# Performance work log

Hardware: AMD Instinct MI355X
Metric: run time of the kernel (lower is better)

Reference implementation:

```python
import jax, jax.numpy as jnp
import numpy as np

B, S, F, D, H, L = 32, 512, 40, 512, 8, 4
T = S + 1
DK, DV = D // 2, D          # expand_k=0.5, expand_v=1.0 (fla GLA defaults)
HK, HV = DK // H, DV // H
GLR = 16                    # gate low-rank dim
GLN = 16.0                  # gate logit normalizer
MLP = 4 * D


def sin_pos(t, d, n=10000.0):
    pos = jnp.arange(t, dtype=jnp.float32)[:, None]
    den = jnp.power(n, 2.0 * jnp.arange(d // 2, dtype=jnp.float32) / d)
    e = jnp.zeros((t, d), jnp.float32)
    e = e.at[:, 0::2].set(jnp.sin(pos / den))
    e = e.at[:, 1::2].set(jnp.cos(pos / den))
    return e


def layernorm(x, w, b, eps=1e-5):
    m = x.mean(-1, keepdims=True)
    v = ((x - m) ** 2).mean(-1, keepdims=True)
    return (x - m) * jax.lax.rsqrt(v + eps) * w + b


def bin_norm(x, l1, b1, l2, b2, y1, y2):
    # x: (b, f, s). BiN: temporal z-norm with per-feature affine (X2) +
    # feature z-norm with per-time affine (X1); unbiased std, small std -> 1.
    st = jnp.sqrt(x.var(axis=2, ddof=1, keepdims=True))
    st = jnp.where(st < 1e-4, 1.0, st)
    Z2 = (x - x.mean(axis=2, keepdims=True)) / st
    X2 = l2[None, :, None] * Z2 + b2[None, :, None]
    sf = jnp.sqrt(x.var(axis=1, ddof=1, keepdims=True))
    sf = jnp.where(sf < 1e-4, 1.0, sf)
    Z1 = (x - x.mean(axis=1, keepdims=True)) / sf
    X1 = l1[None, None, :] * Z1 + b1[None, None, :]
    return y1 * X1 + y2 * X2


def gla_attn(x, qw, kw, vw, gw, gkw1, gkw2, gkb2, gnw, ow):
    # Gated linear attention, recurrent form: S_t = exp(gk_t) * S_{t-1} + k_t v_t^T
    b, t, _ = x.shape
    q = (x @ qw).reshape(b, t, H, HK) * (HK ** -0.5)
    k = (x @ kw).reshape(b, t, H, HK)
    v = (x @ vw).reshape(b, t, H, HV)
    g = (x @ gw).reshape(b, t, H, HV)
    gk = (jax.nn.log_sigmoid((x @ gkw1) @ gkw2 + gkb2) / GLN).reshape(b, t, H, HK)

    def step(Sc, inp):
        qt, kt, vt, gt = inp                       # (b,H,HK),(b,H,HK),(b,H,HV),(b,H,HK)
        Sc = Sc * jnp.exp(gt)[..., None] + kt[..., None] * vt[..., None, :]
        return Sc, jnp.einsum('bhk,bhkv->bhv', qt, Sc)

    init = jnp.zeros((b, H, HK, HV), x.dtype)
    to_t = lambda a: jnp.swapaxes(a, 0, 1)        # (t, b, H, dim)
    _, o = jax.lax.scan(step, init, (to_t(q), to_t(k), to_t(v), to_t(gk)))
    o = jnp.swapaxes(o, 0, 1)                     # (b, t, H, HV)
    o = o * jax.lax.rsqrt((o * o).mean(-1, keepdims=True) + 1e-5) * gnw  # head RMSNorm
    o = o * g * jax.nn.sigmoid(g)                 # swish output gate
    return o.reshape(b, t, DV) @ ow


def setup_inputs():
    key = jax.random.key(0)
    ks = iter(jax.random.split(key, 64))
    r = lambda shape, s=0.02: jax.random.normal(next(ks), shape, jnp.float32) * s
    return dict(
        x=jax.random.normal(next(ks), (B, S, F), jnp.float32),
        bin_l1=r((S,), 0.1), bin_b1=jnp.zeros((S,), jnp.float32),
        bin_l2=r((F,), 0.1), bin_b2=jnp.zeros((F,), jnp.float32),
        bin_y1=jnp.float32(0.5), bin_y2=jnp.float32(0.5),
        emb_w=r((F, D)), emb_b=jnp.zeros((D,), jnp.float32),
        cls_token=jnp.zeros((D,), jnp.float32),
        ln1_w=jnp.ones((L, D), jnp.float32), ln1_b=jnp.zeros((L, D), jnp.float32),
        q_w=r((L, D, DK)), k_w=r((L, D, DK)), v_w=r((L, D, DV)), g_w=r((L, D, DV)),
        gk_w1=r((L, D, GLR)), gk_w2=r((L, GLR, DK)), gk_b2=jnp.zeros((L, DK), jnp.float32),
        gnorm_w=jnp.ones((L, HV), jnp.float32),
        o_w=r((L, DV, D)),
        ln2_w=jnp.ones((L, D), jnp.float32), ln2_b=jnp.zeros((L, D), jnp.float32),
        mlp_w1=r((L, D, MLP)), mlp_b1=jnp.zeros((L, MLP), jnp.float32),
        mlp_w2=r((L, MLP, D)), mlp_b2=jnp.zeros((L, D), jnp.float32),
        head_w=r((D, 3)), head_b=jnp.zeros((3,), jnp.float32),
    )


def reference(x, bin_l1, bin_b1, bin_l2, bin_b2, bin_y1, bin_y2, emb_w, emb_b,
              cls_token, ln1_w, ln1_b, q_w, k_w, v_w, g_w, gk_w1, gk_w2, gk_b2,
              gnorm_w, o_w, ln2_w, ln2_b, mlp_w1, mlp_b1, mlp_w2, mlp_b2,
              head_w, head_b):
    h = bin_norm(jnp.swapaxes(x, 1, 2), bin_l1, bin_b1, bin_l2, bin_b2, bin_y1, bin_y2)
    h = jnp.swapaxes(h, 1, 2) @ emb_w + emb_b                    # (b, s, D)
    cls = jnp.broadcast_to(cls_token, (h.shape[0], 1, D))
    h = jnp.concatenate([h, cls], axis=1) + sin_pos(T, D)[None]  # (b, s+1, D)
    for i in range(L):
        a = gla_attn(layernorm(h, ln1_w[i], ln1_b[i]), q_w[i], k_w[i], v_w[i],
                     g_w[i], gk_w1[i], gk_w2[i], gk_b2[i], gnorm_w[i], o_w[i])
        h = h + a
        m = layernorm(h, ln2_w[i], ln2_b[i])
        m = jax.nn.gelu(m @ mlp_w1[i] + mlp_b1[i], approximate=False)
        h = h + m @ mlp_w2[i] + mlp_b2[i]
    return h[:, -1] @ head_w + head_b                            # (b, 3)
```

## Files before the change

### kernel.cpp

```cpp
#include <hip/hip_runtime.h>
#include <hip/hip_bf16.h>
#include <hip/hip_fp16.h>
#include <math.h>

#define Bsz   32
#define Ssz   512
#define Fsz   40
#define Dsz   512
#define Hh    8
#define Lnum  4
#define Tsz   513
#define DKsz  256
#define DVsz  512
#define HKsz  32
#define HVsz  64
#define Msz   (Bsz*Tsz)
#define Mpad  16512
#define MLPsz 2048
#define NCH   16
#define CSZ   33
#define QKVG  1536
#define VOFFH 8404992

typedef __attribute__((ext_vector_type(4))) float f32x4;
typedef __attribute__((ext_vector_type(8))) short bf16x8;

__device__ __forceinline__ float bf2f(short s) {
  unsigned int u = ((unsigned int)(unsigned short)s) << 16;
  return __builtin_bit_cast(float, u);
}
__device__ __forceinline__ short f2bf(float f) {
  __hip_bfloat16 b = __float2bfloat16(f);
  return __builtin_bit_cast(short, b);
}

__device__ __forceinline__ float wave_sum(float v) {
#pragma unroll
  for (int off = 32; off > 0; off >>= 1) v += __shfl_xor(v, off, 64);
  return v;
}

__global__ void pos_kernel(float* __restrict__ pos) {
  int idx = blockIdx.x * 256 + threadIdx.x;
  if (idx >= Tsz * Dsz) return;
  int t = idx / Dsz, d = idx % Dsz;
  float e = (float)(2 * (d >> 1)) / (float)Dsz;
  float den = powf(10000.f, e);
  float a = (float)t / den;
  pos[idx] = (d & 1) ? cosf(a) : sinf(a);
}

__global__ void tstat_kernel(const float* __restrict__ x,
                             float* __restrict__ mt, float* __restrict__ rst) {
  int bf = blockIdx.x;
  int b = bf / Fsz, f = bf % Fsz;
  int lane = threadIdx.x;
  const float* xp = x + (size_t)b * Ssz * Fsz + f;
  float s = 0.f, sq = 0.f;
  for (int i = lane; i < Ssz; i += 64) {
    float v = xp[(size_t)i * Fsz];
    s += v; sq += v * v;
  }
  s = wave_sum(s); sq = wave_sum(sq);
  if (lane == 0) {
    float m = s / (float)Ssz;
    float var = (sq - (float)Ssz * m * m) / (float)(Ssz - 1);
    float st = sqrtf(fmaxf(var, 0.f));
    if (st < 1e-4f) st = 1.f;
    mt[bf] = m;
    rst[bf] = 1.f / st;
  }
}

__global__ __launch_bounds__(64) void binorm_kernel(
    const float* __restrict__ x, const float* __restrict__ l1,
    const float* __restrict__ b1, const float* __restrict__ l2,
    const float* __restrict__ b2, const float* __restrict__ y1p,
    const float* __restrict__ y2p, const float* __restrict__ mt,
    const float* __restrict__ rst, float* __restrict__ xbT) {
  int row = blockIdx.x;
  int lane = threadIdx.x;
  int b = row / Tsz, t = row % Tsz;
  bool valid = (row < Msz) && (t < Ssz);
  if (!valid) {
    if (lane < Fsz) xbT[(size_t)lane * Mpad + row] = 0.f;
    return;
  }
  float xv = 0.f;
  const float* xp = x + ((size_t)b * Ssz + t) * Fsz;
  if (lane < Fsz) xv = xp[lane];
  float s  = wave_sum(lane < Fsz ? xv : 0.f);
  float sq = wave_sum(lane < Fsz ? xv * xv : 0.f);
  float m = s / (float)Fsz;
  float var = (sq - (float)Fsz * m * m) / (float)(Fsz - 1);
  float sf = sqrtf(fmaxf(var, 0.f));
  if (sf < 1e-4f) sf = 1.f;
  if (lane < Fsz) {
    float y1 = y1p[0], y2 = y2p[0];
    float z1 = (xv - m) / sf;
    float X1 = l1[t] * z1 + b1[t];
    int bf = b * Fsz + lane;
    float z2 = (xv - mt[bf]) * rst[bf];
    float X2 = l2[lane] * z2 + b2[lane];
    xbT[(size_t)lane * Mpad + row] = y1 * X1 + y2 * X2;
  }
}

__global__ __launch_bounds__(256, 4) void embgemm_kernel(
    const float* __restrict__ xbT, const float* __restrict__ emb_w,
    const float* __restrict__ emb_b, const float* __restrict__ cls,
    const float* __restrict__ pos, float* __restrict__ h) {
  __shared__ float as[Fsz][64];
  __shared__ float bs[Fsz][64];
  int tid = threadIdx.x, tx = tid & 15, ty = tid >> 4;
  int r0 = blockIdx.x * 64, c0 = blockIdx.y * 64;
  for (int idx = tid; idx < Fsz * 64; idx += 256) {
    int f = idx >> 6, r = idx & 63;
    as[f][r] = xbT[(size_t)f * Mpad + r0 + r];
    bs[f][r] = emb_w[f * Dsz + c0 + r];
  }
  __syncthreads();
  float acc[4][4] = {};
#pragma unroll 5
  for (int f = 0; f < Fsz; ++f) {
    float4 a = *(const float4*)&as[f][ty * 4];
    float4 bv = *(const float4*)&bs[f][tx * 4];
    float av[4] = {a.x, a.y, a.z, a.w};
    float bw[4] = {bv.x, bv.y, bv.z, bv.w};
#pragma unroll
    for (int i = 0; i < 4; ++i)
#pragma unroll
      for (int j = 0; j < 4; ++j) acc[i][j] += av[i] * bw[j];
  }
#pragma unroll
  for (int i = 0; i < 4; ++i) {
    int gm = r0 + ty * 4 + i;
    int t = gm % Tsz;
    const float* pp = pos + (size_t)t * Dsz;
    bool iscls = (t == Ssz);
    int gn = c0 + tx * 4;
#pragma unroll
    for (int j = 0; j < 4; ++j) {
      float v = iscls ? (cls[gn + j] + pp[gn + j])
                      : (acc[i][j] + emb_b[gn + j] + pp[gn + j]);
      h[(size_t)gm * Dsz + gn + j] = v;
    }
  }
}

__global__ __launch_bounds__(64) void ln_kernel(
    const float* __restrict__ in, const float* __restrict__ w,
    const float* __restrict__ b, short* __restrict__ out) {
  int row = blockIdx.x, lane = threadIdx.x;
  const float* p = in + (size_t)row * Dsz;
  float4 v0 = *(const float4*)(p + lane * 8);
  float4 v1 = *(const float4*)(p + lane * 8 + 4);
  float s  = v0.x + v0.y + v0.z + v0.w + v1.x + v1.y + v1.z + v1.w;
  float sq = v0.x*v0.x + v0.y*v0.y + v0.z*v0.z + v0.w*v0.w
           + v1.x*v1.x + v1.y*v1.y + v1.z*v1.z + v1.w*v1.w;
  s = wave_sum(s); sq = wave_sum(sq);
  float m = s * (1.f / Dsz);
  float var = sq * (1.f / Dsz) - m * m;
  float r = rsqrtf(var + 1e-5f);
  float4 w0 = *(const float4*)(w + lane * 8);
  float4 w1 = *(const float4*)(w + lane * 8 + 4);
  float4 b0 = *(const float4*)(b + lane * 8);
  float4 b1v = *(const float4*)(b + lane * 8 + 4);
  bf16x8 pk;
  pk[0] = f2bf((v0.x - m) * r * w0.x + b0.x);
  pk[1] = f2bf((v0.y - m) * r * w0.y + b0.y);
  pk[2] = f2bf((v0.z - m) * r * w0.z + b0.z);
  pk[3] = f2bf((v0.w - m) * r * w0.w + b0.w);
  pk[4] = f2bf((v1.x - m) * r * w1.x + b1v.x);
  pk[5] = f2bf((v1.y - m) * r * w1.y + b1v.y);
  pk[6] = f2bf((v1.z - m) * r * w1.z + b1v.z);
  pk[7] = f2bf((v1.w - m) * r * w1.w + b1v.w);
  *(bf16x8*)(out + (size_t)row * Dsz + lane * 8) = pk;
}

__global__ __launch_bounds__(256) void wtall_kernel(
    const float* __restrict__ qw, const float* __restrict__ kw,
    const float* __restrict__ vw, const float* __restrict__ gw,
    const float* __restrict__ ow, const float* __restrict__ m1w,
    const float* __restrict__ m2w, short* __restrict__ qkvT,
    short* __restrict__ owT, short* __restrict__ m1T, short* __restrict__ m2T) {
  __shared__ float t[32][33];
  int bid = blockIdx.x;
  int tx = threadIdx.x & 31, ty = threadIdx.x >> 5;
  const float* W; short* Wt; int K, N, k0, n0, nD;
  if (bid < 768) {
    int kx = bid & 15, ny = bid >> 4;
    int n0g = ny * 32;
    int ld;
    if (n0g < 256)       { W = qw; n0 = n0g;        ld = DKsz; }
    else if (n0g < 512)  { W = kw; n0 = n0g - 256;  ld = DKsz; }
    else if (n0g < 1024) { W = vw; n0 = n0g - 512;  ld = DVsz; }
    else                 { W = gw; n0 = n0g - 1024; ld = DVsz; }
    k0 = kx * 32; K = Dsz; N = ld; Wt = qkvT; nD = n0g;
  } else if (bid < 1024) {
    int idx = bid - 768;
    k0 = (idx & 15) * 32; n0 = (idx >> 4) * 32;
    W = ow; Wt = owT; K = DVsz; N = Dsz; nD = n0;
  } else if (bid < 2048) {
    int idx = bid - 1024;
    k0 = (idx & 15) * 32; n0 = (idx >> 4) * 32;
    W = m1w; Wt = m1T; K = Dsz; N = MLPsz; nD = n0;
  } else {
    int idx = bid - 2048;
    k0 = (idx & 63) * 32; n0 = (idx >> 6) * 32;
    W = m2w; Wt = m2T; K = MLPsz; N = Dsz; nD = n0;
  }
#pragma unroll
  for (int r = 0; r < 32; r += 8)
    t[ty + r][tx] = W[(size_t)(k0 + ty + r) * N + n0 + tx];
  __syncthreads();
#pragma unroll
  for (int r = 0; r < 32; r += 8)
    Wt[(size_t)(nD + ty + r) * K + k0 + tx] = f2bf(t[tx][ty + r]);
}

template<int ACT, int OBF, int SCAT, int TN>
__global__ __launch_bounds__(256) void mgemm_kernel(
    const short* __restrict__ A, const short* __restrict__ Bt,
    void* __restrict__ Cv, const float* __restrict__ bias,
    const float* __restrict__ resid, int N, int K) {
  constexpr int MI = (TN == 128) ? 4 : 2;
  __shared__ short As[128 * 64];
  __shared__ short Bs[TN * 64];
  int tid = threadIdx.x;
  int lane = tid & 63, wid = tid >> 6;
  int wrr = (TN == 128) ? (wid >> 1) : wid;
  int wcc = (TN == 128) ? (wid & 1) : 0;

  int Ny = N / TN;
  int total = 129 * Ny;
  int q = total >> 3, r = total & 7;
  int xcd = blockIdx.x & 7, bi = blockIdx.x >> 3;
  int s = xcd * q + (xcd < r ? xcd : r);
  int w = s + bi;
  int m0 = (w / Ny) * 128, n0 = (w % Ny) * TN;

  f32x4 acc[MI][4];
#pragma unroll
  for (int i = 0; i < MI; ++i)
#pragma unroll
    for (int j = 0; j < 4; ++j) acc[i][j] = (f32x4){0.f, 0.f, 0.f, 0.f};

  int kq = lane >> 4;
  int rsel = lane & 15;

  for (int kt = 0; kt < K; kt += 64) {
#pragma unroll
    for (int i = 0; i < 4; ++i) {
      int li = i * 256 + tid;
      int row = li >> 3;
      int gsrc = (li & 7) ^ (row & 7);
      const short* ga = A + (size_t)(m0 + row) * K + kt + gsrc * 8;
      int base = (i * 256 + wid * 64) * 8;
      __builtin_amdgcn_global_load_lds(
          (const __attribute__((address_space(1))) unsigned int*)ga,
          (__attribute__((address_space(3))) unsigned int*)&As[base], 16, 0, 0);
    }
#pragma unroll
    for (int i = 0; i < TN / 32; ++i) {
      int li = i * 256 + tid;
      int row = li >> 3;
      int gsrc = (li & 7) ^ (row & 7);
      const short* gb = Bt + (size_t)(n0 + row) * K + kt + gsrc * 8;
      int base = (i * 256 + wid * 64) * 8;
      __builtin_amdgcn_global_load_lds(
          (const __attribute__((address_space(1))) unsigned int*)gb,
          (__attribute__((address_space(3))) unsigned int*)&Bs[base], 16, 0, 0);
    }
    __syncthreads();
#pragma unroll
    for (int s2 = 0; s2 < 2; ++s2) {
      bf16x8 af[MI], bfr[4];
#pragma unroll
      for (int i = 0; i < MI; ++i) {
        int row = wrr * (MI * 16) + i * 16 + rsel;
        int slot = (s2 * 4 + kq) ^ (row & 7);
        af[i] = *(const bf16x8*)&As[row * 64 + slot * 8];
      }
#pragma unroll
      for (int j = 0; j < 4; ++j) {
        int col = wcc * 64 + j * 16 + rsel;
        int slotB = (s2 * 4 + kq) ^ (col & 7);
        bfr[j] = *(const bf16x8*)&Bs[col * 64 + slotB * 8];
      }
#pragma unroll
      for (int i = 0; i < MI; ++i)
#pragma unroll
        for (int j = 0; j < 4; ++j)
          acc[i][j] = __builtin_amdgcn_mfma_f32_16x16x32_bf16(af[i], bfr[j], acc[i][j], 0, 0, 0);
    }
    __syncthreads();
  }

#pragma unroll
  for (int i = 0; i < MI; ++i) {
    int rbase = m0 + wrr * (MI * 16) + i * 16 + (lane >> 4) * 4;
#pragma unroll
    for (int j = 0; j < 4; ++j) {
      int gn = n0 + wcc * 64 + j * 16 + (lane & 15);
      float bv = (SCAT == 0 && bias) ? bias[gn] : 0.f;
#pragma unroll
      for (int r2 = 0; r2 < 4; ++r2) {
        int gm = rbase + r2;
        float v = acc[i][j][r2] + bv;
        if (SCAT == 0) {
          if (ACT == 1) v = 0.5f * v * (1.f + erff(v * 0.70710678118654752f));
          if (resid) v += resid[(size_t)gm * N + gn];
          if (OBF) ((short*)Cv)[(size_t)gm * N + gn] = f2bf(v);
          else     ((float*)Cv)[(size_t)gm * N + gn] = v;
        } else {
          if (gm < Msz) {
            int bq = gm / Tsz, tq = gm - bq * Tsz;
            if (gn < 512) {
              int hq = (gn >> 5) & 7;
              int off = (gn & 31) | ((gn & 256) >> 3);
              ((__half*)Cv)[(((size_t)bq * 8 + hq) * Tsz + tq) * 64 + off] = __float2half(v);
            } else if (gn < 1024) {
              int hq = (gn >> 6) & 7;
              ((__half*)Cv)[(size_t)VOFFH + (((size_t)bq * 8 + hq) * Tsz + tq) * 64 + (gn & 63)] = __float2half(v);
            } else {
              int hq = (gn >> 6) & 7;
              ((__half*)const_cast<float*>(resid))[(((size_t)bq * 8 + hq) * Tsz + tq) * 64 + (gn & 63)] = __float2half(v);
            }
          }
        }
      }
    }
  }
}

__global__ __launch_bounds__(64) void gk12_kernel(const short* __restrict__ xn,
    const float* __restrict__ w1, const float* __restrict__ w2,
    const float* __restrict__ b2, float* __restrict__ gkeP) {
  int m = blockIdx.x, lane = threadIdx.x;
  __shared__ float xr[512];
  __shared__ float y[16];
  bf16x8 v = *(const bf16x8*)(xn + (size_t)m * Dsz + lane * 8);
#pragma unroll
  for (int e = 0; e < 8; ++e) xr[lane * 8 + e] = bf2f(v[e]);
  __syncthreads();
  int c = lane & 15, q = lane >> 4;
  float acc = 0.f;
#pragma unroll 8
  for (int i = 0; i < 128; ++i) {
    int k = q * 128 + i;
    acc += xr[k] * w1[k * 16 + c];
  }
  acc += __shfl_xor(acc, 16, 64);
  acc += __shfl_xor(acc, 32, 64);
  if (lane < 16) y[c] = acc;
  __syncthreads();
  int b = m / Tsz, t = m - b * Tsz;
#pragma unroll
  for (int p = 0; p < 4; ++p) {
    int n = lane + p * 64;
    float z = b2[n];
#pragma unroll
    for (int r = 0; r < 16; ++r) z += y[r] * w2[r * 256 + n];
    float ls = (z >= 0.f) ? -log1pf(expf(-z)) : z - log1pf(expf(z));
    int hq = n >> 5;
    gkeP[(((size_t)b * 8 + hq) * Tsz + t) * 32 + (n & 31)] = expf(ls * 0.0625f);
  }
}

__global__ __launch_bounds__(64) void scanA_kernel(
    const __half* __restrict__ qkPh, const float* __restrict__ gkeP,
    float* __restrict__ Ac, float* __restrict__ Bc) {
  int gid = blockIdx.x;
  int bh = gid >> 4, c = gid & 15;
  int lane = threadIdx.x;
  int t0 = c * CSZ;
  int nst = min(CSZ, Tsz - t0);
  __shared__ __align__(16) __half s_k[CSZ * 32];
  __shared__ __align__(16) float  s_g[CSZ * 32];
  __shared__ __align__(16) __half s_v[CSZ * 64];
  const size_t rowbase = (size_t)bh * Tsz + t0;
  const __half* qksrc = qkPh + rowbase * 64;
  const __half* vsrc  = qkPh + (size_t)VOFFH + rowbase * 64;
  const float* gsrc   = gkeP + rowbase * 32;
  int nkh = nst * 4;
#pragma unroll
  for (int i = 0; i < 3; ++i) {
    int gi = i * 64 + lane;
    if (gi < nkh) {
      int st = gi >> 2, gq = (gi & 3) * 8;
      __builtin_amdgcn_global_load_lds(
        (const __attribute__((address_space(1))) unsigned int*)(qksrc + (size_t)st * 64 + 32 + gq),
        (__attribute__((address_space(3))) unsigned int*)(s_k + i * 512), 16, 0, 0);
    }
  }
  int ng = nst * 8;
#pragma unroll
  for (int i = 0; i < 5; ++i) {
    int gi = i * 64 + lane;
    if (gi < ng) {
      __builtin_amdgcn_global_load_lds(
        (const __attribute__((address_space(1))) unsigned int*)(gsrc + (size_t)gi * 4),
        (__attribute__((address_space(3))) unsigned int*)(s_g + i * 256), 16, 0, 0);
      __builtin_amdgcn_global_load_lds(
        (const __attribute__((address_space(1))) unsigned int*)(vsrc + (size_t)gi * 8),
        (__attribute__((address_space(3))) unsigned int*)(s_v + i * 512), 16, 0, 0);
    }
  }
  float S[32];
#pragma unroll
  for (int i = 0; i < 32; ++i) S[i] = 0.f;
  float ac = 1.f;
  __syncthreads();
  for (int ts = 0; ts < nst; ++ts) {
    float vv = __half2float(s_v[ts * 64 + lane]);
    const __half2* kp = (const __half2*)&s_k[ts * 32];
#pragma unroll
    for (int j = 0; j < 8; ++j) {
      float4 gg = *(const float4*)&s_g[ts * 32 + j * 4];
      float2 k01 = __half22float2(kp[2 * j]);
      float2 k23 = __half22float2(kp[2 * j + 1]);
      S[4*j+0] = S[4*j+0] * gg.x + k01.x * vv;
      S[4*j+1] = S[4*j+1] * gg.y + k01.y * vv;
      S[4*j+2] = S[4*j+2] * gg.z + k23.x * vv;
      S[4*j+3] = S[4*j+3] * gg.w + k23.y * vv;
    }
    ac *= s_g[ts * 32 + (lane & 31)];
  }
  float* bp = Bc + ((size_t)gid * 64 + lane) * 32;
#pragma unroll
  for (int j = 0; j < 8; ++j)
    *(float4*)(bp + j * 4) = make_float4(S[4*j+0], S[4*j+1], S[4*j+2], S[4*j+3]);
  if (lane < 32) Ac[(size_t)gid * 32 + lane] = ac;
}

__global__ __launch_bounds__(64) void scanB_kernel(
    const float* __restrict__ Ac, float* __restrict__ Bc) {
  int bh = blockIdx.x;
  int lane = threadIdx.x;
  float cur[32];
#pragma unroll
  for (int i = 0; i < 32; ++i) cur[i] = 0.f;
  __shared__ float sA[32];
  for (int c = 0; c < NCH; ++c) {
    size_t gid = (size_t)bh * NCH + c;
    float* bp = Bc + (gid * 64 + lane) * 32;
    __syncthreads();
    if (lane < 32) sA[lane] = Ac[gid * 32 + lane];
    __syncthreads();
    float4 tb[8];
#pragma unroll
    for (int j = 0; j < 8; ++j) tb[j] = *(const float4*)(bp + j * 4);
#pragma unroll
    for (int j = 0; j < 8; ++j)
      *(float4*)(bp + j * 4) = make_float4(cur[4*j+0], cur[4*j+1], cur[4*j+2], cur[4*j+3]);
#pragma unroll
    for (int j = 0; j < 8; ++j) {
      cur[4*j+0] = sA[4*j+0] * cur[4*j+0] + tb[j].x;
      cur[4*j+1] = sA[4*j+1] * cur[4*j+1] + tb[j].y;
      cur[4*j+2] = sA[4*j+2] * cur[4*j+2] + tb[j].z;
      cur[4*j+3] = sA[4*j+3] * cur[4*j+3] + tb[j].w;
    }
  }
}

__global__ __launch_bounds__(64) void scanC_kernel(
    const __half* __restrict__ qkPh, const __half* __restrict__ gP,
    const float* __restrict__ gkeP, const float* __restrict__ gnw,
    const float* __restrict__ Bc, short* __restrict__ att) {
  int gid = blockIdx.x;
  int bh = gid >> 4, c = gid & 15;
  int b = bh >> 3, hh = bh & 7;
  int lane = threadIdx.x;
  int t0 = c * CSZ;
  int nst = min(CSZ, Tsz - t0);
  __shared__ __align__(16) __half s_qk[CSZ * 64];
  __shared__ __align__(16) float  s_g[CSZ * 32];
  __shared__ __align__(16) __half s_v[CSZ * 64];
  __shared__ __align__(16) __half s_gt[CSZ * 64];
  const size_t rowbase = (size_t)bh * Tsz + t0;
  const __half* qksrc = qkPh + rowbase * 64;
  const __half* vsrc  = qkPh + (size_t)VOFFH + rowbase * 64;
  const float* gsrc   = gkeP + rowbase * 32;
  const __half* gtsrc = gP + rowbase * 64;
  int ng = nst * 8;
#pragma unroll
  for (int i = 0; i < 5; ++i) {
    int gi = i * 64 + lane;
    if (gi < ng) {
      __builtin_amdgcn_global_load_lds(
        (const __attribute__((address_space(1))) unsigned int*)(qksrc + (size_t)gi * 8),
        (__attribute__((address_space(3))) unsigned int*)(s_qk + i * 512), 16, 0, 0);
      __builtin_amdgcn_global_load_lds(
        (const __attribute__((address_space(1))) unsigned int*)(vsrc + (size_t)gi * 8),
        (__attribute__((address_space(3))) unsigned int*)(s_v + i * 512), 16, 0, 0);
      __builtin_amdgcn_global_load_lds(
        (const __attribute__((address_space(1))) unsigned int*)(gsrc + (size_t)gi * 4),
        (__attribute__((address_space(3))) unsigned int*)(s_g + i * 256), 16, 0, 0);
      __builtin_amdgcn_global_load_lds(
        (const __attribute__((address_space(1))) unsigned int*)(gtsrc + (size_t)gi * 8),
        (__attribute__((address_space(3))) unsigned int*)(s_gt + i * 512), 16, 0, 0);
    }
  }
  float S[32];
  const float* sp = Bc + ((size_t)gid * 64 + lane) * 32;
#pragma unroll
  for (int j = 0; j < 8; ++j) {
    float4 sv4 = *(const float4*)(sp + j * 4);
    S[4*j+0] = sv4.x; S[4*j+1] = sv4.y; S[4*j+2] = sv4.z; S[4*j+3] = sv4.w;
  }
  float gn = gnw[lane];
  __syncthreads();
  for (int ts = 0; ts < nst; ++ts) {
    float vv = __half2float(s_v[ts * 64 + lane]);
    float gv = __half2float(s_gt[ts * 64 + lane]);
    const __half2* qp = (const __half2*)&s_qk[ts * 64];
    const __half2* kp = qp + 16;
    float o = 0.f;
#pragma unroll
    for (int j = 0; j < 8; ++j) {
      float4 gg = *(const float4*)&s_g[ts * 32 + j * 4];
      float2 q01 = __half22float2(qp[2 * j]);
      float2 q23 = __half22float2(qp[2 * j + 1]);
      float2 k01 = __half22float2(kp[2 * j]);
      float2 k23 = __half22float2(kp[2 * j + 1]);
      S[4*j+0] = S[4*j+0] * gg.x + k01.x * vv;  o += q01.x * S[4*j+0];
      S[4*j+1] = S[4*j+1] * gg.y + k01.y * vv;  o += q01.y * S[4*j+1];
      S[4*j+2] = S[4*j+2] * gg.z + k23.x * vv;  o += q23.x * S[4*j+2];
      S[4*j+3] = S[4*j+3] * gg.w + k23.y * vv;  o += q23.y * S[4*j+3];
    }
    o *= 0.17677669529663689f;
    float ss = wave_sum(o * o);
    float r = rsqrtf(ss * (1.f / 64.f) + 1e-5f);
    float sig = 1.f / (1.f + expf(-gv));
    att[((size_t)b * Tsz + t0 + ts) * DVsz + hh * HVsz + lane] = f2bf(o * r * gn * gv * sig);
  }
}

__global__ __launch_bounds__(64) void head_kernel(
    const float* __restrict__ h, const float* __restrict__ hw,
    const float* __restrict__ hb, float* __restrict__ out) {
  int b = blockIdx.x, lane = threadIdx.x;
  const float* p = h + ((size_t)b * Tsz + Ssz) * Dsz;
  float p0 = 0.f, p1 = 0.f, p2 = 0.f;
#pragma unroll
  for (int j = 0; j < 8; ++j) {
    int d = lane + j * 64;
    float hv = p[d];
    p0 += hv * hw[d * 3 + 0];
    p1 += hv * hw[d * 3 + 1];
    p2 += hv * hw[d * 3 + 2];
  }
  p0 = wave_sum(p0); p1 = wave_sum(p1); p2 = wave_sum(p2);
  if (lane == 0) {
    out[b * 3 + 0] = p0 + hb[0];
    out[b * 3 + 1] = p1 + hb[1];
    out[b * 3 + 2] = p2 + hb[2];
  }
}

extern "C" void kernel_launch(void* const* d_in, const int* in_sizes, int n_in,
                              void* d_out, int out_size, void* d_ws, size_t ws_size,
                              hipStream_t stream) {
  const float* x       = (const float*)d_in[0];
  const float* bin_l1  = (const float*)d_in[1];
  const float* bin_b1  = (const float*)d_in[2];
  const float* bin_l2  = (const float*)d_in[3];
  const float* bin_b2  = (const float*)d_in[4];
  const float* bin_y1  = (const float*)d_in[5];
  const float* bin_y2  = (const float*)d_in[6];
  const float* emb_w   = (const float*)d_in[7];
  const float* emb_b   = (const float*)d_in[8];
  const float* cls     = (const float*)d_in[9];
  const float* ln1_w   = (const float*)d_in[10];
  const float* ln1_b   = (const float*)d_in[11];
  const float* q_w     = (const float*)d_in[12];
  const float* k_w     = (const float*)d_in[13];
  const float* v_w     = (const float*)d_in[14];
  const float* g_w     = (const float*)d_in[15];
  const float* gk_w1   = (const float*)d_in[16];
  const float* gk_w2   = (const float*)d_in[17];
  const float* gk_b2   = (const float*)d_in[18];
  const float* gnorm_w = (const float*)d_in[19];
  const float* o_w     = (const float*)d_in[20];
  const float* ln2_w   = (const float*)d_in[21];
  const float* ln2_b   = (const float*)d_in[22];
  const float* mlp_w1  = (const float*)d_in[23];
  const float* mlp_b1  = (const float*)d_in[24];
  const float* mlp_w2  = (const float*)d_in[25];
  const float* mlp_b2  = (const float*)d_in[26];
  const float* head_w  = (const float*)d_in[27];
  const float* head_b  = (const float*)d_in[28];
  float* out = (float*)d_out;

  char* wptr = (char*)d_ws;
  auto alloc = [&](size_t bytes) { char* p = wptr; wptr += (bytes + 255) & ~(size_t)255; return p; };
  float* pos  = (float*)alloc((size_t)Tsz * Dsz * 4);
  float* h    = (float*)alloc((size_t)Mpad * Dsz * 4);
  short* xn   = (short*)alloc((size_t)Mpad * Dsz * 2);
  float* qkP  = (float*)alloc((size_t)Mpad * MLPsz * 2);
  float* gkeP = (float*)alloc((size_t)256 * Tsz * 32 * 4);
  __half* gP  = (__half*)alloc((size_t)256 * Tsz * 64 * 2);
  float* mt   = (float*)alloc((size_t)Bsz * Fsz * 4);
  float* rst  = (float*)alloc((size_t)Bsz * Fsz * 4);
  float* Ac   = (float*)alloc((size_t)Bsz * Hh * NCH * 32 * 4);
  float* Bc   = (float*)alloc((size_t)Bsz * Hh * NCH * 64 * 32 * 4);
  short* wtr  = (short*)alloc((size_t)3145728 * 2);
  float* xbT  = qkP;
  short* mid  = (short*)qkP;
  short* att  = xn;
  __half* qkPh = (__half*)qkP;

  short* qkvT = wtr;
  short* owT  = qkvT + 786432;
  short* m1T  = owT + 262144;
  short* m2T  = m1T + 1048576;

  hipLaunchKernelGGL(pos_kernel, dim3((Tsz * Dsz + 255) / 256), dim3(256), 0, stream, pos);
  hipLaunchKernelGGL(tstat_kernel, dim3(Bsz * Fsz), dim3(64), 0, stream, x, mt, rst);
  hipLaunchKernelGGL(binorm_kernel, dim3(Mpad), dim3(64), 0, stream,
                     x, bin_l1, bin_b1, bin_l2, bin_b2, bin_y1, bin_y2, mt, rst, xbT);
  hipLaunchKernelGGL(embgemm_kernel, dim3(258, 8), dim3(256), 0, stream,
                     xbT, emb_w, emb_b, cls, pos, h);

  dim3 blk256(256);
  for (int l = 0; l < Lnum; ++l) {
    hipLaunchKernelGGL(wtall_kernel, dim3(3072), blk256, 0, stream,
                       q_w + (size_t)l*Dsz*DKsz, k_w + (size_t)l*Dsz*DKsz,
                       v_w + (size_t)l*Dsz*DVsz, g_w + (size_t)l*Dsz*DVsz,
                       o_w + (size_t)l*DVsz*Dsz, mlp_w1 + (size_t)l*Dsz*MLPsz,
                       mlp_w2 + (size_t)l*MLPsz*Dsz, qkvT, owT, m1T, m2T);

    const float* lw1 = ln1_w + l * Dsz;  const float* lb1 = ln1_b + l * Dsz;
    const float* g1w = gk_w1 + (size_t)l * Dsz * 16;
    const float* g2w = gk_w2 + (size_t)l * 16 * DKsz;
    const float* g2b = gk_b2 + (size_t)l * DKsz;
    const float* gnw = gnorm_w + l * HVsz;
    const float* lw2 = ln2_w + l * Dsz;  const float* lb2 = ln2_b + l * Dsz;
    const float* m1b = mlp_b1 + (size_t)l * MLPsz;
    const float* m2b = mlp_b2 + (size_t)l * Dsz;

    hipLaunchKernelGGL(ln_kernel, dim3(Msz), dim3(64), 0, stream, h, lw1, lb1, xn);

    hipLaunchKernelGGL((mgemm_kernel<0,0,1,128>), dim3(129 * 12), blk256, 0, stream,
                       xn, qkvT, (void*)qkPh, (const float*)nullptr, (const float*)gP, QKVG, Dsz);
    hipLaunchKernelGGL(gk12_kernel, dim3(Msz), dim3(64), 0, stream, xn, g1w, g2w, g2b, gkeP);

    hipLaunchKernelGGL(scanA_kernel, dim3(Bsz * Hh * NCH), dim3(64), 0, stream,
                       qkPh, gkeP, Ac, Bc);
    hipLaunchKernelGGL(scanB_kernel, dim3(Bsz * Hh), dim3(64), 0, stream, Ac, Bc);
    hipLaunchKernelGGL(scanC_kernel, dim3(Bsz * Hh * NCH), dim3(64), 0, stream,
                       qkPh, gP, gkeP, gnw, Bc, att);

    hipLaunchKernelGGL((mgemm_kernel<0,0,0,64>), dim3(129 * 8), blk256, 0, stream,
                       att, owT, (void*)h, (const float*)nullptr, h, Dsz, DVsz);

    hipLaunchKernelGGL(ln_kernel, dim3(Msz), dim3(64), 0, stream, h, lw2, lb2, xn);
    hipLaunchKernelGGL((mgemm_kernel<1,1,0,128>), dim3(129 * 16), blk256, 0, stream,
                       xn, m1T, (void*)mid, m1b, (const float*)nullptr, MLPsz, Dsz);
    hipLaunchKernelGGL((mgemm_kernel<0,0,0,64>), dim3(129 * 8), blk256, 0, stream,
                       mid, m2T, (void*)h, m2b, h, Dsz, MLPsz);
  }

  hipLaunchKernelGGL(head_kernel, dim3(Bsz), dim3(64), 0, stream, h, head_w, head_b, out);
}
```

Baseline: 1.576 ms.

## Double scan chunk count, store chunk states in fp16 inside spare buffer

The chunked GLA scan now uses 32 chunks of 17 steps instead of 16 chunks of 33, which doubles block-level parallelism in the intra-chunk passes and halves their serial length. The scanB pass across chunks gets twice as many sequential steps. Inter-chunk state buffers move to fp16 and live in unused space of the qkP workspace, halving their traffic. The output dot product is split into four partial accumulators to shorten the dependency chain. Storing carried states in fp16 risks precision loss or overflow.

```diff
diff --git a/kernel.cpp b/kernel.cpp
--- a/kernel.cpp
+++ b/kernel.cpp
@@ -17,8 +17,8 @@
 #define Msz   (Bsz*Tsz)
 #define Mpad  16512
 #define MLPsz 2048
-#define NCH   16
-#define CSZ   33
+#define NCH   32
+#define CSZ   17
 #define QKVG  1536
 #define VOFFH 8404992
 
@@ -370,9 +370,9 @@
 
 __global__ __launch_bounds__(64) void scanA_kernel(
     const __half* __restrict__ qkPh, const float* __restrict__ gkeP,
-    float* __restrict__ Ac, float* __restrict__ Bc) {
+    float* __restrict__ Ac, __half* __restrict__ Bc) {
   int gid = blockIdx.x;
-  int bh = gid >> 4, c = gid & 15;
+  int bh = gid >> 5, c = gid & 31;
   int lane = threadIdx.x;
   int t0 = c * CSZ;
   int nst = min(CSZ, Tsz - t0);
@@ -385,7 +385,7 @@
   const float* gsrc   = gkeP + rowbase * 32;
   int nkh = nst * 4;
 #pragma unroll
-  for (int i = 0; i < 3; ++i) {
+  for (int i = 0; i < 2; ++i) {
     int gi = i * 64 + lane;
     if (gi < nkh) {
       int st = gi >> 2, gq = (gi & 3) * 8;
@@ -396,7 +396,7 @@
   }
   int ng = nst * 8;
 #pragma unroll
-  for (int i = 0; i < 5; ++i) {
+  for (int i = 0; i < 3; ++i) {
     int gi = i * 64 + lane;
     if (gi < ng) {
       __builtin_amdgcn_global_load_lds(
@@ -427,15 +427,19 @@
     }
     ac *= s_g[ts * 32 + (lane & 31)];
   }
-  float* bp = Bc + ((size_t)gid * 64 + lane) * 32;
-#pragma unroll
-  for (int j = 0; j < 8; ++j)
-    *(float4*)(bp + j * 4) = make_float4(S[4*j+0], S[4*j+1], S[4*j+2], S[4*j+3]);
+  __half* bp = Bc + ((size_t)gid * 64 + lane) * 32;
+#pragma unroll
+  for (int j = 0; j < 8; ++j) {
+    __half2 h01 = __floats2half2_rn(S[4*j+0], S[4*j+1]);
+    __half2 h23 = __floats2half2_rn(S[4*j+2], S[4*j+3]);
+    *(__half2*)(bp + j * 4)     = h01;
+    *(__half2*)(bp + j * 4 + 2) = h23;
+  }
   if (lane < 32) Ac[(size_t)gid * 32 + lane] = ac;
 }
 
 __global__ __launch_bounds__(64) void scanB_kernel(
-    const float* __restrict__ Ac, float* __restrict__ Bc) {
+    const float* __restrict__ Ac, __half* __restrict__ Bc) {
   int bh = blockIdx.x;
   int lane = threadIdx.x;
   float cur[32];
@@ -444,32 +448,34 @@
   __shared__ float sA[32];
   for (int c = 0; c < NCH; ++c) {
     size_t gid = (size_t)bh * NCH + c;
-    float* bp = Bc + (gid * 64 + lane) * 32;
+    __half* bp = Bc + (gid * 64 + lane) * 32;
     __syncthreads();
     if (lane < 32) sA[lane] = Ac[gid * 32 + lane];
     __syncthreads();
-    float4 tb[8];
-#pragma unroll
-    for (int j = 0; j < 8; ++j) tb[j] = *(const float4*)(bp + j * 4);
-#pragma unroll
-    for (int j = 0; j < 8; ++j)
-      *(float4*)(bp + j * 4) = make_float4(cur[4*j+0], cur[4*j+1], cur[4*j+2], cur[4*j+3]);
+    float tb[32];
 #pragma unroll
     for (int j = 0; j < 8; ++j) {
-      cur[4*j+0] = sA[4*j+0] * cur[4*j+0] + tb[j].x;
-      cur[4*j+1] = sA[4*j+1] * cur[4*j+1] + tb[j].y;
-      cur[4*j+2] = sA[4*j+2] * cur[4*j+2] + tb[j].z;
-      cur[4*j+3] = sA[4*j+3] * cur[4*j+3] + tb[j].w;
-    }
+      float2 t01 = __half22float2(*(const __half2*)(bp + j * 4));
+      float2 t23 = __half22float2(*(const __half2*)(bp + j * 4 + 2));
+      tb[4*j+0] = t01.x; tb[4*j+1] = t01.y; tb[4*j+2] = t23.x; tb[4*j+3] = t23.y;
+    }
+#pragma unroll
+    for (int j = 0; j < 8; ++j) {
+      *(__half2*)(bp + j * 4)     = __floats2half2_rn(cur[4*j+0], cur[4*j+1]);
+      *(__half2*)(bp + j * 4 + 2) = __floats2half2_rn(cur[4*j+2], cur[4*j+3]);
+    }
+#pragma unroll
+    for (int i = 0; i < 32; ++i)
+      cur[i] = sA[i] * cur[i] + tb[i];
   }
 }
 
 __global__ __launch_bounds__(64) void scanC_kernel(
     const __half* __restrict__ qkPh, const __half* __restrict__ gP,
     const float* __restrict__ gkeP, const float* __restrict__ gnw,
-    const float* __restrict__ Bc, short* __restrict__ att) {
+    const __half* __restrict__ Bc, short* __restrict__ att) {
   int gid = blockIdx.x;
-  int bh = gid >> 4, c = gid & 15;
+  int bh = gid >> 5, c = gid & 31;
   int b = bh >> 3, hh = bh & 7;
   int lane = threadIdx.x;
   int t0 = c * CSZ;
@@ -485,7 +491,7 @@
   const __half* gtsrc = gP + rowbase * 64;
   int ng = nst * 8;
 #pragma unroll
-  for (int i = 0; i < 5; ++i) {
+  for (int i = 0; i < 3; ++i) {
     int gi = i * 64 + lane;
     if (gi < ng) {
       __builtin_amdgcn_global_load_lds(
@@ -503,11 +509,12 @@
     }
   }
   float S[32];
-  const float* sp = Bc + ((size_t)gid * 64 + lane) * 32;
+  const __half* sp = Bc + ((size_t)gid * 64 + lane) * 32;
 #pragma unroll
   for (int j = 0; j < 8; ++j) {
-    float4 sv4 = *(const float4*)(sp + j * 4);
-    S[4*j+0] = sv4.x; S[4*j+1] = sv4.y; S[4*j+2] = sv4.z; S[4*j+3] = sv4.w;
+    float2 s01 = __half22float2(*(const __half2*)(sp + j * 4));
+    float2 s23 = __half22float2(*(const __half2*)(sp + j * 4 + 2));
+    S[4*j+0] = s01.x; S[4*j+1] = s01.y; S[4*j+2] = s23.x; S[4*j+3] = s23.y;
   }
   float gn = gnw[lane];
   __syncthreads();
@@ -516,7 +523,7 @@
     float gv = __half2float(s_gt[ts * 64 + lane]);
     const __half2* qp = (const __half2*)&s_qk[ts * 64];
     const __half2* kp = qp + 16;
-    float o = 0.f;
+    float o0 = 0.f, o1 = 0.f, o2 = 0.f, o3 = 0.f;
 #pragma unroll
     for (int j = 0; j < 8; ++j) {
       float4 gg = *(const float4*)&s_g[ts * 32 + j * 4];
@@ -524,12 +531,12 @@
       float2 q23 = __half22float2(qp[2 * j + 1]);
       float2 k01 = __half22float2(kp[2 * j]);
       float2 k23 = __half22float2(kp[2 * j + 1]);
-      S[4*j+0] = S[4*j+0] * gg.x + k01.x * vv;  o += q01.x * S[4*j+0];
-      S[4*j+1] = S[4*j+1] * gg.y + k01.y * vv;  o += q01.y * S[4*j+1];
-      S[4*j+2] = S[4*j+2] * gg.z + k23.x * vv;  o += q23.x * S[4*j+2];
-      S[4*j+3] = S[4*j+3] * gg.w + k23.y * vv;  o += q23.y * S[4*j+3];
-    }
-    o *= 0.17677669529663689f;
+      S[4*j+0] = S[4*j+0] * gg.x + k01.x * vv;  o0 += q01.x * S[4*j+0];
+      S[4*j+1] = S[4*j+1] * gg.y + k01.y * vv;  o1 += q01.y * S[4*j+1];
+      S[4*j+2] = S[4*j+2] * gg.z + k23.x * vv;  o2 += q23.x * S[4*j+2];
+      S[4*j+3] = S[4*j+3] * gg.w + k23.y * vv;  o3 += q23.y * S[4*j+3];
+    }
+    float o = ((o0 + o1) + (o2 + o3)) * 0.17677669529663689f;
     float ss = wave_sum(o * o);
     float r = rsqrtf(ss * (1.f / 64.f) + 1e-5f);
     float sig = 1.f / (1.f + expf(-gv));
@@ -604,12 +611,12 @@
   float* mt   = (float*)alloc((size_t)Bsz * Fsz * 4);
   float* rst  = (float*)alloc((size_t)Bsz * Fsz * 4);
   float* Ac   = (float*)alloc((size_t)Bsz * Hh * NCH * 32 * 4);
-  float* Bc   = (float*)alloc((size_t)Bsz * Hh * NCH * 64 * 32 * 4);
   short* wtr  = (short*)alloc((size_t)3145728 * 2);
   float* xbT  = qkP;
   short* mid  = (short*)qkP;
   short* att  = xn;
   __half* qkPh = (__half*)qkP;
+  __half* Bc  = qkPh + (size_t)2 * VOFFH;
 
   short* qkvT = wtr;
   short* owT  = qkvT + 786432;
```

Result: no change. 1.581 ms (+0.4%).
